# Kernel optimization log

Hardware: AMD Instinct MI355X
Metric: run time of the kernel (lower is better)

Reference implementation:

```python
import jax, jax.numpy as jnp
import numpy as np

R = 2           # local_radius
N_HEADS = 4     # num_heads
OUT = 256       # out_channels


def _attn_scale(x, Wq, bq, Wk, bk, Wv, bv):
    # Faithful jax port of SparseSelfAttention.forward
    B, C, H, W = x.shape
    N = H * W
    d = OUT // N_HEADS
    # torch x.view(B, N, -1) on contiguous [B,C,H,W] == row-major reshape
    xf = x.reshape(B, N, C)
    q = (xf @ Wq.T + bq).reshape(B, N, N_HEADS, d).transpose(0, 2, 1, 3)  # [B,h,N,d]
    k = (xf @ Wk.T + bk).reshape(B, N, N_HEADS, d).transpose(0, 2, 1, 3)
    v = (xf @ Wv.T + bv).reshape(B, N, N_HEADS, d).transpose(0, 2, 1, 3)
    scale = 1.0 / np.sqrt(OUT).astype(np.float32)
    acc = jnp.zeros_like(v)
    for dh in range(-R, R + 1):
        for dw in range(-R, R + 1):
            # original rolls dims (-3,-2) of [B,h,N,d] -> (head, point) dims
            rk = jnp.roll(k, (dh, dw), axis=(1, 2))
            s = jnp.einsum('bhnd,bhmd->bhnm', q, rk) * scale  # [B,h,N,N]
            a = jax.nn.softmax(s, axis=-1)                     # dropout p=0.0
            rv = jnp.roll(v, (-dh, -dw), axis=(1, 2))
            acc = acc + jnp.einsum('bhnm,bhmd->bhnd', a, rv)
    return acc.transpose(0, 2, 1, 3).reshape(B, N, OUT)  # [B,N,out]


def setup_inputs() -> dict:
    key = jax.random.key(0)
    ks = jax.random.split(key, 8)
    B, C, H, W = 2, 256, 32, 32
    std = 1.0 / np.sqrt(C)
    d = {
        'x0': jax.random.normal(ks[0], (B, C, H, W), jnp.float32),
        'x1': jax.random.normal(ks[1], (B, C, H, W), jnp.float32),
    }
    i = 2
    for s in (0, 1):
        for p in ('q', 'k', 'v'):
            d[f'W{p}{s}'] = jax.random.uniform(ks[i], (OUT, C), jnp.float32, -std, std)
            d[f'b{p}{s}'] = jnp.zeros((OUT,), jnp.float32)
            i += 1
    return d


def reference(x0, x1, Wq0, bq0, Wk0, bk0, Wv0, bv0,
              Wq1, bq1, Wk1, bk1, Wv1, bv1):
    out0 = _attn_scale(x0, Wq0, bq0, Wk0, bk0, Wv0, bv0)
    out1 = _attn_scale(x1, Wq1, bq1, Wk1, bk1, Wv1, bv1)
    return out0 + out1  # [B, N, out_channels], summed across scales
```

## Files before the change

kernel.cpp:

```cpp
#include <hip/hip_runtime.h>
#include <hip/hip_bf16.h>


typedef __bf16 bf16x8 __attribute__((ext_vector_type(8)));
typedef __bf16 bf16x4 __attribute__((ext_vector_type(4)));
typedef float f32x4 __attribute__((ext_vector_type(4)));

#define MFMA16(A,B,C) __builtin_amdgcn_mfma_f32_16x16x32_bf16(A,B,C,0,0,0)

__device__ __forceinline__ bf16x8 ld8(const __bf16* p){ return *reinterpret_cast<const bf16x8*>(p); }

struct ProjArgs { const float* W[6]; const float* Bz[6]; };

__global__ __launch_bounds__(256) void cvt_k(const float* __restrict__ x0,
                                             const float* __restrict__ x1,
                                             ProjArgs args,
                                             __bf16* __restrict__ Xb,
                                             __bf16* __restrict__ Wb)
{
    int g = blockIdx.x*256 + threadIdx.x;
    const float* src; __bf16* dst;
    if (g < 131072){
        int s = g >> 16;
        int E = (g & 65535)*8;
        int blk = E >> 9, lane8 = (E >> 3) & 63;
        int row = (blk>>3)*16 + (lane8 & 15);
        int ci  = (blk&7)*32 + (lane8>>4)*8;
        src = (s ? x1 : x0) + (size_t)row*256 + ci;
        dst = Xb + (size_t)s*524288 + E;
    } else {
        int gw = g - 131072;
        int sp = gw >> 13;
        int E = (gw & 8191)*8;
        int blk = E >> 9, lane8 = (E >> 3) & 63;
        int co = (blk>>3)*16 + (lane8 & 15);
        int ci = (blk&7)*32 + (lane8>>4)*8;
        src = args.W[sp] + (size_t)co*256 + ci;
        dst = Wb + (size_t)sp*65536 + E;
    }
    f32x4 a = *reinterpret_cast<const f32x4*>(src);
    f32x4 b = *reinterpret_cast<const f32x4*>(src+4);
    bf16x8 o;
    #pragma unroll
    for (int j=0;j<4;j++){ o[j] = (__bf16)a[j]; o[4+j] = (__bf16)b[j]; }
    *reinterpret_cast<bf16x8*>(dst) = o;
}

__global__ __launch_bounds__(256) void proj_k(const __bf16* __restrict__ Xb,
                                              const __bf16* __restrict__ Wb,
                                              ProjArgs args,
                                              __bf16* __restrict__ Qb,
                                              __bf16* __restrict__ Kb,
                                              __bf16* __restrict__ Vb)
{
    int bid = blockIdx.x;
    int cg = bid % 12, rg = bid / 12;
    int tid = threadIdx.x, wv = tid >> 6, l = tid & 63;
    int lr = l & 15, lg = l >> 4;
    int s = rg >> 5;
    const __bf16* Xf = Xb + (size_t)s*524288;
    int p = cg >> 2;
    const __bf16* Wf = Wb + (size_t)(s*3+p)*65536;
    const float* bp = args.Bz[s*3 + p];
    int rowbase = rg*64 + wv*16;
    int colbase = (cg & 3)*64;
    int rowblk = ((rg & 31)*4 + wv);

    f32x4 acc[4];
    #pragma unroll
    for (int t=0;t<4;t++) acc[t] = f32x4{0.f,0.f,0.f,0.f};

    #pragma unroll
    for (int kk=0; kk<8; kk++){
        bf16x8 af = ld8(Xf + (size_t)(rowblk*8 + kk)*512 + l*8);
        #pragma unroll
        for (int ct=0; ct<4; ct++){
            bf16x8 bfv = ld8(Wf + (size_t)(((cg&3)*4 + ct)*8 + kk)*512 + l*8);
            acc[ct] = MFMA16(af, bfv, acc[ct]);
        }
    }
    if (p < 2){
        __bf16* dst = (p==0) ? Qb : Kb;
        float qs = (p==0) ? 0.09016844136f : 1.0f;
        #pragma unroll
        for (int ct=0; ct<4; ct++){
            int co = colbase + ct*16 + lr;
            float bias = bp[co];
            int h = co >> 6, d = co & 63;
            #pragma unroll
            for (int i=0;i<4;i++){
                int gr = rowbase + lg*4 + i;
                int b = (gr >> 10) & 1, n = gr & 1023;
                size_t base = ((size_t)(s*2+b)*4 + h)*65536;
                size_t off = (size_t)(n>>4)*1024 + (size_t)(d>>5)*512
                           + ((d>>3)&3)*128 + (n&15)*8 + (d&7);
                dst[base + off] = (__bf16)((acc[ct][i] + bias)*qs);
            }
        }
    } else {
        #pragma unroll
        for (int ct=0; ct<4; ct++){
            int co = colbase + ct*16 + lr;
            float bias = bp[co];
            int h = co >> 6, d = co & 63;
            #pragma unroll
            for (int i=0;i<4;i++){
                int gr = rowbase + lg*4 + i;
                int b = (gr >> 10) & 1, n = gr & 1023;
                size_t idx = ((((size_t)s*2 + b)*4 + h)*1024 + n)*64 + d;
                Vb[idx] = (__bf16)(acc[ct][i] + bias);
            }
        }
    }
}

__global__ __launch_bounds__(256) void smooth_k(const __bf16* __restrict__ Vb,
                                                __bf16* __restrict__ WT)
{
    __shared__ __bf16 Vt[72][66];
    int bid = blockIdx.x;
    int sbu = bid >> 4, n0 = (bid & 15)*64;
    int tid = threadIdx.x;
    const __bf16* Vs = Vb + (size_t)sbu*65536;
    for (int idx = tid; idx < 576; idx += 256){
        int row = idx >> 3, ch = idx & 7;
        int n = (n0 - 4 + row) & 1023;
        bf16x8 v = ld8(Vs + (size_t)n*64 + ch*8);
        #pragma unroll
        for (int j=0;j<8;j++) Vt[row][ch*8+j] = v[j];
    }
    __syncthreads();
    int w = tid >> 6, l = tid & 63;
    __bf16* dst = WT + (size_t)sbu*65536;
    int m = n0 + l;
    int kb = m >> 5, m32 = m & 31;
    int p = (m32 < 16) ? ((m32>>2)*8 + (m32&3))
                       : (((m32-16)>>2)*8 + 4 + (m32&3));
    size_t pbase = (size_t)kb*2048 + (p>>3)*128 + (p&7);
    #pragma unroll
    for (int it=0; it<16; it++){
        int d = it*4 + w;
        float sum = 0.f;
        #pragma unroll
        for (int j=0;j<5;j++) sum += (float)Vt[l + j*2][d];
        dst[pbase + (size_t)(d>>4)*512 + (d&15)*8] = (__bf16)sum;
    }
}

__global__ __launch_bounds__(256) void attn_k(const __bf16* __restrict__ Qb,
                                              const __bf16* __restrict__ Kb,
                                              const __bf16* __restrict__ WT,
                                              __bf16* __restrict__ pvp,
                                              float* __restrict__ dsp,
                                              int KS, int kslog, int kpc)
{
    int tid = threadIdx.x, wv = tid>>6, l = tid&63, lr = l&15, lg = l>>4;
    int t = blockIdx.x;
    int qg = t & 7; t >>= 3;
    int kc = t & (KS-1); t >>= kslog;
    int dhi = t & 3, h = (t>>2)&3, b = (t>>4)&1, s = (t>>5)&1;
    int dhv = (dhi==2) ? -1 : (dhi==3 ? 2 : dhi);
    int g = (h - dhv + 4) & 3;
    int u = (h + dhv + 4) & 3;
    int sb = s*2 + b;
    int nbase = qg*128 + wv*32;
    const __bf16* Qw = Qb + ((size_t)(sb*4 + h))*65536 + (size_t)(nbase>>4)*1024;
    const __bf16* Kg = Kb + ((size_t)(sb*4 + g))*65536;
    const __bf16* Wu = WT + ((size_t)(sb*4 + u))*65536;
    bf16x8 qa0 = ld8(Qw + l*8),        qa1 = ld8(Qw + 512 + l*8);
    bf16x8 qb0 = ld8(Qw + 1024 + l*8), qb1 = ld8(Qw + 1536 + l*8);

    const f32x4 z = {0.f,0.f,0.f,0.f};
    f32x4 pvA[4] = {z,z,z,z};
    f32x4 pvB[4] = {z,z,z,z};
    float dsA = 0.f, dsB = 0.f;

    int kbeg = kc * kpc, kend = kbeg + kpc;
    for (int kt=kbeg; kt<kend; kt+=32){
        const __bf16* k0 = Kg + (size_t)(kt>>4)*1024 + l*8;
        bf16x8 kf00 = ld8(k0),        kf01 = ld8(k0 + 512);
        bf16x8 kf10 = ld8(k0 + 1024), kf11 = ld8(k0 + 1536);
        const __bf16* w0 = Wu + (size_t)(kt>>5)*2048 + l*8;
        bf16x8 wd0 = ld8(w0);
        bf16x8 wd1 = ld8(w0 + 512);
        bf16x8 wd2 = ld8(w0 + 1024);
        bf16x8 wd3 = ld8(w0 + 1536);
        f32x4 sA0 = MFMA16(kf00, qa0, z); sA0 = MFMA16(kf01, qa1, sA0);
        f32x4 sA1 = MFMA16(kf10, qa0, z); sA1 = MFMA16(kf11, qa1, sA1);
        f32x4 sB0 = MFMA16(kf00, qb0, z); sB0 = MFMA16(kf01, qb1, sB0);
        f32x4 sB1 = MFMA16(kf10, qb0, z); sB1 = MFMA16(kf11, qb1, sB1);
        bf16x8 paA, paB;
        #pragma unroll
        for (int i=0;i<4;i++){
            float eA0 = __builtin_amdgcn_exp2f(sA0[i]);
            float eA1 = __builtin_amdgcn_exp2f(sA1[i]);
            float eB0 = __builtin_amdgcn_exp2f(sB0[i]);
            float eB1 = __builtin_amdgcn_exp2f(sB1[i]);
            dsA += eA0 + eA1;
            dsB += eB0 + eB1;
            paA[i] = (__bf16)eA0; paA[4+i] = (__bf16)eA1;
            paB[i] = (__bf16)eB0; paB[4+i] = (__bf16)eB1;
        }
        pvA[0] = MFMA16(wd0, paA, pvA[0]);
        pvA[1] = MFMA16(wd1, paA, pvA[1]);
        pvA[2] = MFMA16(wd2, paA, pvA[2]);
        pvA[3] = MFMA16(wd3, paA, pvA[3]);
        pvB[0] = MFMA16(wd0, paB, pvB[0]);
        pvB[1] = MFMA16(wd1, paB, pvB[1]);
        pvB[2] = MFMA16(wd2, paB, pvB[2]);
        pvB[3] = MFMA16(wd3, paB, pvB[3]);
    }
    dsA += __shfl_xor(dsA, 16, 64); dsA += __shfl_xor(dsA, 32, 64);
    dsB += __shfl_xor(dsB, 16, 64); dsB += __shfl_xor(dsB, 32, 64);

    int slot = (s*4 + dhi)*KS + kc;
    __bf16* pp = pvp + (size_t)slot*524288;
    #pragma unroll
    for (int dt=0; dt<4; dt++){
        bf16x4 oA, oB;
        #pragma unroll
        for (int i=0;i<4;i++){ oA[i] = (__bf16)pvA[dt][i]; oB[i] = (__bf16)pvB[dt][i]; }
        size_t col = (size_t)h*64 + dt*16 + lg*4;
        *reinterpret_cast<bf16x4*>(pp + ((size_t)b*1024 + nbase + lr)*256 + col)      = oA;
        *reinterpret_cast<bf16x4*>(pp + ((size_t)b*1024 + nbase + 16 + lr)*256 + col) = oB;
    }
    if (l < 16){
        dsp[(size_t)slot*8192 + ((size_t)b*4+h)*1024 + nbase + l]      = dsA;
        dsp[(size_t)slot*8192 + ((size_t)b*4+h)*1024 + nbase + 16 + l] = dsB;
    }
}

__global__ __launch_bounds__(256) void reduce_k(const __bf16* __restrict__ pvp,
                                                const float* __restrict__ dsp,
                                                float* __restrict__ out, int KS)
{
    int idx = blockIdx.x*256 + threadIdx.x;
    int c8 = idx & 31, bn = idx >> 5;
    int h = c8 >> 3;
    size_t dsoff = (size_t)(bn>>10)*4096 + (size_t)h*1024 + (bn & 1023);
    float acc[8] = {0,0,0,0,0,0,0,0};
    for (int s4=0; s4<8; s4++){
        float wgt = ((s4&3)==3) ? 2.f : 1.f;
        float fsum[8] = {0,0,0,0,0,0,0,0};
        float DS = 0.f;
        for (int kc=0; kc<KS; kc++){
            int slot = s4*KS + kc;
            bf16x8 v = ld8(pvp + (size_t)slot*524288 + (size_t)bn*256 + c8*8);
            #pragma unroll
            for (int j=0;j<8;j++) fsum[j] += (float)v[j];
            DS += dsp[(size_t)slot*8192 + dsoff];
        }
        float sc = wgt / DS;
        #pragma unroll
        for (int j=0;j<8;j++) acc[j] += fsum[j]*sc;
    }
    f32x4 o0 = {acc[0],acc[1],acc[2],acc[3]};
    f32x4 o1 = {acc[4],acc[5],acc[6],acc[7]};
    *reinterpret_cast<f32x4*>(out + (size_t)idx*8)     = o0;
    *reinterpret_cast<f32x4*>(out + (size_t)idx*8 + 4) = o1;
}

extern "C" void kernel_launch(void* const* d_in, const int* in_sizes, int n_in,
                              void* d_out, int out_size, void* d_ws, size_t ws_size,
                              hipStream_t stream)
{
    const float* x0 = (const float*)d_in[0];
    const float* x1 = (const float*)d_in[1];
    ProjArgs pa;
    for (int s=0;s<2;s++) for (int p=0;p<3;p++){
        pa.W[s*3+p]  = (const float*)d_in[2 + s*6 + p*2];
        pa.Bz[s*3+p] = (const float*)d_in[3 + s*6 + p*2];
    }
    char* wsb = (char*)d_ws;
    __bf16* Qb = (__bf16*)(wsb);
    __bf16* Kb = (__bf16*)(wsb + (2u<<20));
    __bf16* Vb = (__bf16*)(wsb + (4u<<20));
    __bf16* WT = (__bf16*)(wsb + (6u<<20));
    __bf16* Xb = (__bf16*)(wsb + (8u<<20));
    __bf16* Wb = (__bf16*)(wsb + (10u<<20));
    char*   pvb = wsb + (11u<<20);

    size_t base = 11u<<20;
    int KS = 1, kslog = 0;
    if (ws_size >= base + 2*(8u<<20) + 2*(256u<<10)) { KS = 2; kslog = 1; }
    __bf16* pvp = (__bf16*)pvb;
    float*  dsp = (float*)(pvb + (size_t)KS*(8u<<20));
    int kpc = 1024 / KS;

    cvt_k<<<704, 256, 0, stream>>>(x0, x1, pa, Xb, Wb);
    proj_k<<<768, 256, 0, stream>>>(Xb, Wb, pa, Qb, Kb, Vb);
    smooth_k<<<256, 256, 0, stream>>>(Vb, WT);
    attn_k<<<512*KS, 256, 0, stream>>>(Qb, Kb, WT, pvp, dsp, KS, kslog, kpc);
    reduce_k<<<256, 256, 0, stream>>>(pvp, dsp, (float*)d_out, KS);
}
```

Baseline: 55.03 us.

## Stage projection outputs through LDS for vector stores; drop attention key split

The projection kernel now writes its bias-added results into a shared-memory tile in the destination layout, then issues coalesced 16-byte global stores instead of scattered 2-byte stores. The attention kernel also drops the key-split (KS) path and always processes all 1024 keys per block. This halves its grid and the partial buffers, and simplifies the reduce kernel to a single slot per scale and shift. The gain is less partial traffic and reduction work, traded against half the attention parallelism (512 blocks) on a large GPU.

```diff
diff --git a/kernel.cpp b/kernel.cpp
--- a/kernel.cpp
+++ b/kernel.cpp
@@ -53,6 +53,7 @@
                                               __bf16* __restrict__ Kb,
                                               __bf16* __restrict__ Vb)
 {
+    __shared__ __bf16 stage[4096];
     int bid = blockIdx.x;
     int cg = bid % 12, rg = bid / 12;
     int tid = threadIdx.x, wv = tid >> 6, l = tid & 63;
@@ -62,7 +63,6 @@
     int p = cg >> 2;
     const __bf16* Wf = Wb + (size_t)(s*3+p)*65536;
     const float* bp = args.Bz[s*3 + p];
-    int rowbase = rg*64 + wv*16;
     int colbase = (cg & 3)*64;
     int rowblk = ((rg & 31)*4 + wv);
 
@@ -79,39 +79,33 @@
             acc[ct] = MFMA16(af, bfv, acc[ct]);
         }
     }
-    if (p < 2){
-        __bf16* dst = (p==0) ? Qb : Kb;
-        float qs = (p==0) ? 0.09016844136f : 1.0f;
-        #pragma unroll
-        for (int ct=0; ct<4; ct++){
-            int co = colbase + ct*16 + lr;
-            float bias = bp[co];
-            int h = co >> 6, d = co & 63;
-            #pragma unroll
-            for (int i=0;i<4;i++){
-                int gr = rowbase + lg*4 + i;
-                int b = (gr >> 10) & 1, n = gr & 1023;
-                size_t base = ((size_t)(s*2+b)*4 + h)*65536;
-                size_t off = (size_t)(n>>4)*1024 + (size_t)(d>>5)*512
-                           + ((d>>3)&3)*128 + (n&15)*8 + (d&7);
-                dst[base + off] = (__bf16)((acc[ct][i] + bias)*qs);
-            }
+    float qs = (p==0) ? 0.09016844136f : 1.0f;
+    #pragma unroll
+    for (int ct=0; ct<4; ct++){
+        int d = ct*16 + lr;
+        float bias = bp[colbase + d];
+        #pragma unroll
+        for (int i=0;i<4;i++){
+            float v = (acc[ct][i] + bias) * qs;
+            int a;
+            if (p < 2) a = wv*1024 + ((d>>5)&1)*512 + ((d>>3)&3)*128 + (lg*4+i)*8 + (d&7);
+            else       a = (wv*16 + lg*4 + i)*64 + d;
+            stage[a] = (__bf16)v;
         }
-    } else {
-        #pragma unroll
-        for (int ct=0; ct<4; ct++){
-            int co = colbase + ct*16 + lr;
-            float bias = bp[co];
-            int h = co >> 6, d = co & 63;
-            #pragma unroll
-            for (int i=0;i<4;i++){
-                int gr = rowbase + lg*4 + i;
-                int b = (gr >> 10) & 1, n = gr & 1023;
-                size_t idx = ((((size_t)s*2 + b)*4 + h)*1024 + n)*64 + d;
-                Vb[idx] = (__bf16)(acc[ct][i] + bias);
-            }
-        }
-    }
+    }
+    __syncthreads();
+    int gr0 = rg*64;
+    int b = (gr0 >> 10) & 1, n0 = gr0 & 1023;
+    int h = cg & 3;
+    int sb = s*2 + b;
+    __bf16* dstb; size_t goff;
+    if (p == 0){ dstb = Qb; goff = ((size_t)(sb*4 + h))*65536 + (size_t)(n0>>4)*1024; }
+    else if (p == 1){ dstb = Kb; goff = ((size_t)(sb*4 + h))*65536 + (size_t)(n0>>4)*1024; }
+    else { dstb = Vb; goff = ((size_t)(sb*4 + h)*1024 + n0)*64; }
+    bf16x8 v0 = *reinterpret_cast<const bf16x8*>(stage + tid*16);
+    bf16x8 v1 = *reinterpret_cast<const bf16x8*>(stage + tid*16 + 8);
+    *reinterpret_cast<bf16x8*>(dstb + goff + (size_t)tid*16)     = v0;
+    *reinterpret_cast<bf16x8*>(dstb + goff + (size_t)tid*16 + 8) = v1;
 }
 
 __global__ __launch_bounds__(256) void smooth_k(const __bf16* __restrict__ Vb,
@@ -151,13 +145,11 @@
                                               const __bf16* __restrict__ Kb,
                                               const __bf16* __restrict__ WT,
                                               __bf16* __restrict__ pvp,
-                                              float* __restrict__ dsp,
-                                              int KS, int kslog, int kpc)
+                                              float* __restrict__ dsp)
 {
     int tid = threadIdx.x, wv = tid>>6, l = tid&63, lr = l&15, lg = l>>4;
     int t = blockIdx.x;
     int qg = t & 7; t >>= 3;
-    int kc = t & (KS-1); t >>= kslog;
     int dhi = t & 3, h = (t>>2)&3, b = (t>>4)&1, s = (t>>5)&1;
     int dhv = (dhi==2) ? -1 : (dhi==3 ? 2 : dhi);
     int g = (h - dhv + 4) & 3;
@@ -175,8 +167,7 @@
     f32x4 pvB[4] = {z,z,z,z};
     float dsA = 0.f, dsB = 0.f;
 
-    int kbeg = kc * kpc, kend = kbeg + kpc;
-    for (int kt=kbeg; kt<kend; kt+=32){
+    for (int kt=0; kt<1024; kt+=32){
         const __bf16* k0 = Kg + (size_t)(kt>>4)*1024 + l*8;
         bf16x8 kf00 = ld8(k0),        kf01 = ld8(k0 + 512);
         bf16x8 kf10 = ld8(k0 + 1024), kf11 = ld8(k0 + 1536);
@@ -213,7 +204,7 @@
     dsA += __shfl_xor(dsA, 16, 64); dsA += __shfl_xor(dsA, 32, 64);
     dsB += __shfl_xor(dsB, 16, 64); dsB += __shfl_xor(dsB, 32, 64);
 
-    int slot = (s*4 + dhi)*KS + kc;
+    int slot = s*4 + dhi;
     __bf16* pp = pvp + (size_t)slot*524288;
     #pragma unroll
     for (int dt=0; dt<4; dt++){
@@ -232,27 +223,21 @@
 
 __global__ __launch_bounds__(256) void reduce_k(const __bf16* __restrict__ pvp,
                                                 const float* __restrict__ dsp,
-                                                float* __restrict__ out, int KS)
+                                                float* __restrict__ out)
 {
     int idx = blockIdx.x*256 + threadIdx.x;
     int c8 = idx & 31, bn = idx >> 5;
     int h = c8 >> 3;
     size_t dsoff = (size_t)(bn>>10)*4096 + (size_t)h*1024 + (bn & 1023);
     float acc[8] = {0,0,0,0,0,0,0,0};
+    #pragma unroll
     for (int s4=0; s4<8; s4++){
         float wgt = ((s4&3)==3) ? 2.f : 1.f;
-        float fsum[8] = {0,0,0,0,0,0,0,0};
-        float DS = 0.f;
-        for (int kc=0; kc<KS; kc++){
-            int slot = s4*KS + kc;
-            bf16x8 v = ld8(pvp + (size_t)slot*524288 + (size_t)bn*256 + c8*8);
-            #pragma unroll
-            for (int j=0;j<8;j++) fsum[j] += (float)v[j];
-            DS += dsp[(size_t)slot*8192 + dsoff];
-        }
+        bf16x8 v = ld8(pvp + (size_t)s4*524288 + (size_t)bn*256 + c8*8);
+        float DS = dsp[(size_t)s4*8192 + dsoff];
         float sc = wgt / DS;
         #pragma unroll
-        for (int j=0;j<8;j++) acc[j] += fsum[j]*sc;
+        for (int j=0;j<8;j++) acc[j] += (float)v[j] * sc;
     }
     f32x4 o0 = {acc[0],acc[1],acc[2],acc[3]};
     f32x4 o1 = {acc[4],acc[5],acc[6],acc[7]};
@@ -278,18 +263,12 @@
     __bf16* WT = (__bf16*)(wsb + (6u<<20));
     __bf16* Xb = (__bf16*)(wsb + (8u<<20));
     __bf16* Wb = (__bf16*)(wsb + (10u<<20));
-    char*   pvb = wsb + (11u<<20);
-
-    size_t base = 11u<<20;
-    int KS = 1, kslog = 0;
-    if (ws_size >= base + 2*(8u<<20) + 2*(256u<<10)) { KS = 2; kslog = 1; }
-    __bf16* pvp = (__bf16*)pvb;
-    float*  dsp = (float*)(pvb + (size_t)KS*(8u<<20));
-    int kpc = 1024 / KS;
+    __bf16* pvp = (__bf16*)(wsb + (11u<<20));
+    float*  dsp = (float*)(wsb + (19u<<20));
 
     cvt_k<<<704, 256, 0, stream>>>(x0, x1, pa, Xb, Wb);
     proj_k<<<768, 256, 0, stream>>>(Xb, Wb, pa, Qb, Kb, Vb);
     smooth_k<<<256, 256, 0, stream>>>(Vb, WT);
-    attn_k<<<512*KS, 256, 0, stream>>>(Qb, Kb, WT, pvp, dsp, KS, kslog, kpc);
-    reduce_k<<<256, 256, 0, stream>>>(pvp, dsp, (float*)d_out, KS);
-}
+    attn_k<<<512, 256, 0, stream>>>(Qb, Kb, WT, pvp, dsp);
+    reduce_k<<<256, 256, 0, stream>>>(pvp, dsp, (float*)d_out);
+}
```

Measured after the change: 51.73 us. 1.06x faster.
